# Performance work log

Measured on AMD Instinct MI355X. Metric: run time of the kernel, lower is better.

Reference implementation:

```python
import jax, jax.numpy as jnp
import numpy as np

DIM, M_DIM, FOURIER, KNN = 128, 16, 4, 32
EDGE_IN = 2 * FOURIER + 2 * DIM + 1  # 265


def silu(x):
    return x * jax.nn.sigmoid(x)


def setup_inputs() -> dict:
    key = jax.random.key(0)
    ks = jax.random.split(key, 12)
    b, n = 2, 4096

    def w(k, shape):
        return jax.random.normal(k, shape, dtype=jnp.float32) * 0.02

    return {
        "feats": jax.random.normal(ks[0], (b, n, DIM), dtype=jnp.float32),
        "coors": jax.random.normal(ks[1], (b, n, 3), dtype=jnp.float32) * 3.0,
        # edge_mlp: Linear(265, 530) -> SiLU -> Linear(530, 16) -> SiLU
        "We1": w(ks[2], (EDGE_IN, 2 * EDGE_IN)), "be1": jnp.zeros((2 * EDGE_IN,), jnp.float32),
        "We2": w(ks[3], (2 * EDGE_IN, M_DIM)), "be2": jnp.zeros((M_DIM,), jnp.float32),
        # coors_mlp: Linear(16, 64) -> SiLU -> Linear(64, 1)
        "Wc1": w(ks[4], (M_DIM, 4 * M_DIM)), "bc1": jnp.zeros((4 * M_DIM,), jnp.float32),
        "Wc2": w(ks[5], (4 * M_DIM, 1)), "bc2": jnp.zeros((1,), jnp.float32),
        # node_mlp: Linear(dim+16, 2*dim) -> SiLU -> Linear(2*dim, dim)
        "Wn1": w(ks[6], (DIM + M_DIM, 2 * DIM)), "bn1": jnp.zeros((2 * DIM,), jnp.float32),
        "Wn2": w(ks[7], (2 * DIM, DIM)), "bn2": jnp.zeros((DIM,), jnp.float32),
    }


def reference(feats, coors, We1, be1, We2, be2, Wc1, bc1, Wc2, bc2, Wn1, bn1, Wn2, bn2):
    b, n, d = feats.shape
    # pairwise relative coords and squared distance: (b, n, n, 3), (b, n, n)
    rel_coors = coors[:, :, None, :] - coors[:, None, :, :]
    rel_dist = jnp.sum(rel_coors ** 2, axis=-1)

    # k nearest neighbors (smallest distance)
    _, idx = jax.lax.top_k(-rel_dist, KNN)  # (b, n, K)
    rel_coors = jnp.take_along_axis(rel_coors, idx[..., None], axis=2)  # (b, n, K, 3)
    rel_dist = jnp.take_along_axis(rel_dist, idx, axis=2)[..., None]    # (b, n, K, 1)

    # fourier encode distance -> (b, n, K, 2*F + 1)
    scales = 2.0 ** jnp.arange(FOURIER, dtype=rel_dist.dtype)
    xs = rel_dist[..., None] / scales  # (b, n, K, 1, F)
    fe = jnp.concatenate([jnp.sin(xs), jnp.cos(xs), rel_dist[..., None]], axis=-1)
    rel_dist = fe.reshape(b, n, KNN, 2 * FOURIER + 1)

    bidx = jnp.arange(b)[:, None, None]
    feats_j = feats[bidx, idx]                                   # (b, n, K, d)
    feats_i = jnp.broadcast_to(feats[:, :, None, :], (b, n, KNN, d))

    edge_in = jnp.concatenate([feats_i, feats_j, rel_dist], axis=-1)  # (b, n, K, 265)
    m_ij = silu(silu(edge_in @ We1 + be1) @ We2 + be2)                # (b, n, K, m)

    coor_w = (silu(m_ij @ Wc1 + bc1) @ Wc2 + bc2)[..., 0]             # (b, n, K)
    coors_out = jnp.einsum('bij,bijc->bic', coor_w, rel_coors) + coors

    m_i = m_ij.sum(axis=2)                                            # (b, n, m)
    node_h = silu(jnp.concatenate([feats, m_i], axis=-1) @ Wn1 + bn1)
    node_out = node_h @ Wn2 + bn2 + feats
    return node_out, coors_out
```

## Files before the change

kernel.cpp:

```cpp
#include <hip/hip_runtime.h>
#include <hip/hip_bf16.h>
#include <stdint.h>

typedef __hip_bfloat16 bf16;

using sh8    = __attribute__((ext_vector_type(8)))  short;
using sh4    = __attribute__((ext_vector_type(4)))  short;
using us4    = __attribute__((ext_vector_type(4)))  unsigned short;
using f32x16 = __attribute__((ext_vector_type(16))) float;
using fx4    = __attribute__((ext_vector_type(4)))  float;

#define NN    4096
#define NODES 8192
#define DIM   128
#define MD    16
#define KNNK  32
#define H1N   530
#define CPAD  544
#define PROW  1088

#define OFF_W1AB 0
#define OFF_WE2A 8704
#define OFF_WC1A 17536
#define OFF_BE2  19584
#define OFF_BC1  19616
#define OFF_WC2  19744
#define OFF_BC2  19872
#define WIMG_SH  19880

__device__ __forceinline__ float b2f(bf16 x){ return __bfloat162float(x); }
__device__ __forceinline__ bf16  f2b(float x){ return __float2bfloat16(x); }
__device__ __forceinline__ float silu_f(float x){
    return x * __builtin_amdgcn_rcpf(1.f + __expf(-x));
}

__device__ __forceinline__ unsigned short f2us(float f){
    unsigned x = __float_as_uint(f);
    unsigned r = x + 0x7FFFu + ((x >> 16) & 1u);
    return (unsigned short)(r >> 16);
}
__device__ __forceinline__ float us2f(unsigned short u){
    return __uint_as_float(((unsigned)u) << 16);
}
__device__ __forceinline__ unsigned pkbf(float a, float b){
    __hip_bfloat162 v = __float22bfloat162_rn(make_float2(a, b));
    return *(unsigned*)&v;
}

struct Ptrs { const void* p[14]; int n[14]; };

__global__ __launch_bounds__(256) void detect_kernel(Ptrs ps, int* flags){
    int tn = blockIdx.x;
    const bf16* s = (const bf16*)ps.p[tn];
    int n = ps.n[tn]; if (n > 8192) n = 8192;
    int bad = 0;
    for (int i = threadIdx.x; i < n; i += 256){
        float v = b2f(s[i]);
        if (!(fabsf(v) <= 64.f)) bad = 1;
    }
    __shared__ int sbad;
    if (threadIdx.x == 0) sbad = 0;
    __syncthreads();
    if (bad) atomicOr(&sbad, 1);
    __syncthreads();
    if (threadIdx.x == 0) flags[tn] = sbad;
}

struct ConvTab {
    const void* src[14];
    int dstoff[14];
    int prefix[15];
};

__global__ __launch_bounds__(256) void convert_all(ConvTab tab,
                                                   const int* __restrict__ flags,
                                                   float* __restrict__ base){
    int gid = blockIdx.x * 256 + threadIdx.x;
    if (gid >= tab.prefix[14]) return;
    int tn = 0;
    #pragma unroll
    for (int k = 1; k < 14; ++k)
        if (gid >= tab.prefix[k]) tn = k;
    int local = gid - tab.prefix[tn];
    int f = flags[tn];
    float v = f ? ((const float*)tab.src[tn])[local]
                : b2f(((const bf16*)tab.src[tn])[local]);
    base[tab.dstoff[tn] + local] = v;
}

__global__ __launch_bounds__(256) void prep_kernel(
        const float* __restrict__ We1, const float* __restrict__ We2,
        const float* __restrict__ Wc1, const float* __restrict__ be2,
        const float* __restrict__ bc1, const float* __restrict__ Wc2,
        const float* __restrict__ bc2, const float* __restrict__ feats,
        unsigned short* __restrict__ gwimg,
        unsigned short* __restrict__ We1T,
        unsigned short* __restrict__ fBF){
    int gid = blockIdx.x * 256 + threadIdx.x;
    if (gid < 4352){
        int c = gid >> 3, f = gid & 7;
        gwimg[OFF_W1AB + gid] = (c < H1N) ? f2us(We1[(size_t)(256 + f) * H1N + c]) : 0;
    } else if (gid < 8704){
        int e = gid - 4352; int c = e >> 3, jj = e & 7;
        gwimg[OFF_W1AB + 4352 + e] =
            (jj == 0 && c < H1N) ? f2us(We1[(size_t)264 * H1N + c]) : 0;
    } else if (gid < 17536){
        int e = gid - 8704; int o = e / 552, c = e - o * 552;
        gwimg[OFF_WE2A + e] = (c < H1N) ? f2us(We2[(size_t)c * 16 + o]) : 0;
    } else if (gid < 19584){
        int e = gid - 17536; int u = e >> 5, k = e & 31;
        gwimg[OFF_WC1A + e] = (k < 16) ? f2us(Wc1[(size_t)k * 64 + u]) : 0;
    } else if (gid < 19600){
        ((float*)(gwimg + OFF_BE2))[gid - 19584] = be2[gid - 19584];
    } else if (gid < 19664){
        ((float*)(gwimg + OFF_BC1))[gid - 19600] = bc1[gid - 19600];
    } else if (gid < 19728){
        ((float*)(gwimg + OFF_WC2))[gid - 19664] = Wc2[gid - 19664];
    } else if (gid < 19732){
        int z = gid - 19728;
        ((float*)(gwimg + OFF_BC2))[z] = (z == 0) ? bc2[0] : 0.f;
    } else if (gid >= 32768 && gid < 32768 + 1088 * 128){
        int e = gid - 32768; int n = e >> 7, k = e & 127;
        float v;
        if (n < CPAD) v = (n < H1N) ? We1[(size_t)k * H1N + n] : 0.f;
        else { int n2 = n - CPAD; v = (n2 < H1N) ? We1[(size_t)(128 + k) * H1N + n2] : 0.f; }
        We1T[e] = f2us(v);
    } else if (gid >= 172032 && gid < 172032 + NODES * DIM){
        int e = gid - 172032;
        fBF[e] = f2us(feats[e]);
    }
}

__global__ __launch_bounds__(256) void knn_kernel(const float* __restrict__ coors,
                                                  int* __restrict__ idx_out){
    __shared__ unsigned hist[4][1024];
    __shared__ unsigned sBin, sBelow;
    __shared__ unsigned wpart[4];
    __shared__ int  sOcnt;
    __shared__ unsigned long long wred64[4];
    __shared__ unsigned long long sWin64;

    int node = blockIdx.x;
    int b = node >> 12, i = node & (NN - 1);
    const float* cb = coors + (size_t)b * NN * 3;
    int t = threadIdx.x, lane = t & 63, wid = t >> 6;

    float qx = cb[i*3+0], qy = cb[i*3+1], qz = cb[i*3+2];

    unsigned db[16];
    unsigned bk[16];
    #pragma unroll
    for (int s = 0; s < 16; ++s){
        int j = (s << 8) + t;
        float dx = qx - cb[j*3+0];
        float dy = qy - cb[j*3+1];
        float dz = qz - cb[j*3+2];
        float d  = dx*dx + dy*dy + dz*dz;
        float d2 = d * d;
        db[s] = __float_as_uint(d);
        bk[s] = __float_as_uint(d2 * d2) >> 22;
    }

    {
        uint4* hz = (uint4*)hist;
        uint4 z = make_uint4(0,0,0,0);
        #pragma unroll
        for (int e = 0; e < 4; ++e) hz[e * 256 + t] = z;
    }
    __syncthreads();
    #pragma unroll
    for (int s = 0; s < 16; ++s)
        atomicAdd(&hist[wid][bk[s]], 1u);
    if (t == 0) sOcnt = 0;
    __syncthreads();

    unsigned cnt[4]; unsigned S = 0;
    #pragma unroll
    for (int r = 0; r < 4; ++r){
        unsigned c = hist[0][4*t+r] + hist[1][4*t+r] + hist[2][4*t+r] + hist[3][4*t+r];
        cnt[r] = c; S += c;
    }
    unsigned scan = S;
    #pragma unroll
    for (int off = 1; off < 64; off <<= 1){
        unsigned nv = __shfl_up(scan, off);
        if (lane >= off) scan += nv;
    }
    if (lane == 63) wpart[wid] = scan;
    __syncthreads();
    unsigned wbase = 0;
    #pragma unroll
    for (int w = 0; w < 4; ++w)
        if (w < wid) wbase += wpart[w];
    unsigned run = wbase + scan - S;
    #pragma unroll
    for (int r = 0; r < 4; ++r){
        if (run < KNNK && run + cnt[r] >= KNNK){ sBin = 4*t + r; sBelow = run; }
        run += cnt[r];
    }
    __syncthreads();
    unsigned B = sBin, need = KNNK - sBelow;

    #pragma unroll
    for (int s = 0; s < 16; ++s){
        if (bk[s] < B){
            int pos = atomicAdd(&sOcnt, 1);
            idx_out[(size_t)node * KNNK + pos] = (s << 8) + t;
        }
    }
    __syncthreads();
    int C = sOcnt;
    unsigned long long lastk = 0;
    for (unsigned r = 0; r < need; ++r){
        unsigned long long lmin = ~0ull;
        #pragma unroll
        for (int s = 0; s < 16; ++s){
            if (bk[s] == B){
                unsigned long long mk =
                    (((unsigned long long)db[s] << 32) | (unsigned)((s << 8) + t)) + 1ull;
                if (mk > lastk && mk < lmin) lmin = mk;
            }
        }
        #pragma unroll
        for (int off = 32; off > 0; off >>= 1){
            unsigned long long o = __shfl_xor(lmin, off);
            if (o < lmin) lmin = o;
        }
        if (lane == 0) wred64[wid] = lmin;
        __syncthreads();
        if (t == 0){
            unsigned long long m = wred64[0];
            if (wred64[1] < m) m = wred64[1];
            if (wred64[2] < m) m = wred64[2];
            if (wred64[3] < m) m = wred64[3];
            sWin64 = m;
            idx_out[(size_t)node * KNNK + C + r] = (int)(unsigned)((m - 1ull) & 0xffffffffull);
        }
        __syncthreads();
        lastk = sWin64;
    }
}

__global__ __launch_bounds__(256) void p_gemm(const unsigned short* __restrict__ fBF,
                                              const unsigned short* __restrict__ We1T,
                                              const float* __restrict__ be1,
                                              unsigned short* __restrict__ P){
    int t = threadIdx.x, lane = t & 63, wid = t >> 6;
    int e31 = lane & 31, hi = lane >> 5;
    int mW = (blockIdx.x << 7) + (wid << 5);
    int n0 = blockIdx.y << 5;

    const unsigned short* Arow = fBF  + (size_t)(mW + e31) * DIM + hi * 8;
    const unsigned short* Brow = We1T + (size_t)(n0 + e31) * DIM + hi * 8;

    f32x16 acc = {0.f,0.f,0.f,0.f,0.f,0.f,0.f,0.f,0.f,0.f,0.f,0.f,0.f,0.f,0.f,0.f};
    #pragma unroll
    for (int kc = 0; kc < 8; ++kc){
        sh8 a  = *(const sh8*)(Arow + kc * 16);
        sh8 bv = *(const sh8*)(Brow + kc * 16);
        acc = __builtin_amdgcn_mfma_f32_32x32x16_bf16(a, bv, acc, 0, 0, 0);
    }
    int n = n0 + e31;
    float beadd = 0.f;
    if (n < CPAD) beadd = (n < H1N) ? be1[n] : 0.f;
    #pragma unroll
    for (int g = 0; g < 4; ++g)
        #pragma unroll
        for (int r = 0; r < 4; ++r){
            int m = mW + 8*g + 4*hi + r;
            P[(size_t)m * PROW + n] = f2us(acc[4*g + r] + beadd);
        }
}

__global__ __launch_bounds__(512, 6) void edge_kernel(
        const float* __restrict__ coors, const int* __restrict__ idx,
        const unsigned short* __restrict__ gw,
        const unsigned short* __restrict__ P,
        float* __restrict__ mi_out, void* __restrict__ dout,
        const int* __restrict__ flagp){
    __shared__ __align__(16) unsigned short sWe2[16 * 552];
    __shared__ __align__(16) unsigned short trans[8][1280];

    int t = threadIdx.x, lane = t & 63, wid = t >> 6;
    int gnode = (blockIdx.x << 3) + wid;
    int b = gnode >> 12;

    {
        const float4* s1 = (const float4*)(gw + OFF_WE2A);
        float4* d1 = (float4*)sWe2;
        for (int e = t; e < 1104; e += 512) d1[e] = s1[e];
    }

    const float* cb = coors + (size_t)b * NN * 3;
    int i = gnode & (NN - 1);
    float qx = cb[i*3+0], qy = cb[i*3+1], qz = cb[i*3+2];

    int e31 = lane & 31, hi = lane >> 5;
    int e15 = lane & 15, q  = lane >> 4;

    int jme = idx[(size_t)gnode * KNNK + e31];
    float rx = qx - cb[jme*3+0];
    float ry = qy - cb[jme*3+1];
    float rz = qz - cb[jme*3+2];
    float d = rx*rx + ry*ry + rz*rz;

    unsigned frb[9];
    frb[0] = f2us(sinf(d));         frb[1] = f2us(sinf(d * 0.5f));
    frb[2] = f2us(sinf(d * 0.25f)); frb[3] = f2us(sinf(d * 0.125f));
    frb[4] = f2us(cosf(d));         frb[5] = f2us(cosf(d * 0.5f));
    frb[6] = f2us(cosf(d * 0.25f)); frb[7] = f2us(cosf(d * 0.125f));
    frb[8] = f2us(d);

    sh8 bfragC;
    #pragma unroll
    for (int j = 0; j < 8; ++j)
        bfragC[j] = (hi == 0) ? (short)frb[j]
                  : (short)((j == 0) ? frb[8] : (j == 1) ? 0x3F80u : 0u);

    int nbase = gnode & ~(NN - 1);
    int j0 = __shfl(jme, lane >> 2);
    int j1 = __shfl(jme, 16 + (lane >> 2));
    const unsigned short* Pst0 = P + (size_t)(nbase + j0) * PROW + CPAD + (lane & 3) * 8;
    const unsigned short* Pst1 = P + (size_t)(nbase + j1) * PROW + CPAD + (lane & 3) * 8;
    const unsigned short* Pirow = P + (size_t)gnode * PROW;

    unsigned short* stg = &trans[wid][0];
    unsigned short* sw0 = stg + (lane >> 2) * 40 + (lane & 3) * 8;
    unsigned short* sw1 = stg + (16 + (lane >> 2)) * 40 + (lane & 3) * 8;

    const float* g_be2 = (const float*)(gw + OFF_BE2);
    const float* g_bc1 = (const float*)(gw + OFF_BC1);
    const float* g_wc2 = (const float*)(gw + OFF_WC2);
    const float* g_bc2 = (const float*)(gw + OFF_BC2);

    fx4 accD0 = {0.f,0.f,0.f,0.f};
    fx4 accD1 = {0.f,0.f,0.f,0.f};

    __syncthreads();

    for (int ch = 0; ch < 17; ++ch){
        int c0 = ch * 32;
        sh8 g0v = *(const sh8*)(Pst0 + c0);
        sh8 g1v = *(const sh8*)(Pst1 + c0);
        unsigned short piS = Pirow[c0 + e31];
        sh8 afrag = *(const sh8*)(gw + OFF_W1AB + (size_t)(hi * 544 + c0 + e31) * 8);
        afrag[1] = hi ? (short)piS : afrag[1];

        *(sh8*)sw0 = g0v;
        *(sh8*)sw1 = g1v;
        asm volatile("s_waitcnt lgkmcnt(0)" ::: "memory");

        f32x16 cc;
        #pragma unroll
        for (int g = 0; g < 4; ++g){
            us4 pj = *(const us4*)(stg + e31 * 40 + 8*g + 4*hi);
            cc[4*g+0] = us2f(pj.x);
            cc[4*g+1] = us2f(pj.y);
            cc[4*g+2] = us2f(pj.z);
            cc[4*g+3] = us2f(pj.w);
        }
        f32x16 h = __builtin_amdgcn_mfma_f32_32x32x16_bf16(afrag, bfragC, cc, 0, 0, 0);

        #pragma unroll
        for (int g = 0; g < 4; ++g){
            unsigned lo = pkbf(silu_f(h[4*g+0]), silu_f(h[4*g+1]));
            unsigned hi2 = pkbf(silu_f(h[4*g+2]), silu_f(h[4*g+3]));
            *(uint2*)&stg[e31 * 40 + 8*g + 4*hi] = make_uint2(lo, hi2);
        }
        asm volatile("s_waitcnt lgkmcnt(0)" ::: "memory");

        sh8 wa  = *(const sh8*)&sWe2[e15 * 552 + c0 + q * 8];
        sh8 bt0 = *(const sh8*)&stg[e15 * 40 + q * 8];
        sh8 bt1 = *(const sh8*)&stg[(16 + e15) * 40 + q * 8];
        accD0 = __builtin_amdgcn_mfma_f32_16x16x32_bf16(wa, bt0, accD0, 0, 0, 0);
        accD1 = __builtin_amdgcn_mfma_f32_16x16x32_bf16(wa, bt1, accD1, 0, 0, 0);
    }

    fx4 be2q = *(const fx4*)&g_be2[q * 4];
    float msum[4];
    float mv0[4], mv1[4];
    #pragma unroll
    for (int r = 0; r < 4; ++r){
        mv0[r] = silu_f(accD0[r] + be2q[r]);
        mv1[r] = silu_f(accD1[r] + be2q[r]);
        msum[r] = mv0[r] + mv1[r];
    }
    *(uint2*)&stg[e15 * 16 + q * 4] =
        make_uint2(pkbf(mv0[0], mv0[1]), pkbf(mv0[2], mv0[3]));
    *(uint2*)&stg[(16 + e15) * 16 + q * 4] =
        make_uint2(pkbf(mv1[0], mv1[1]), pkbf(mv1[2], mv1[3]));
    #pragma unroll
    for (int r = 0; r < 4; ++r){
        msum[r] += __shfl_xor(msum[r], 1);
        msum[r] += __shfl_xor(msum[r], 2);
        msum[r] += __shfl_xor(msum[r], 4);
        msum[r] += __shfl_xor(msum[r], 8);
    }
    if (e15 == 0){
        fx4 mv = { msum[0], msum[1], msum[2], msum[3] };
        *(fx4*)(mi_out + (size_t)gnode * MD + q * 4) = mv;
    }
    asm volatile("s_waitcnt lgkmcnt(0)" ::: "memory");

    float tsum0 = 0.f, tsum1 = 0.f;
    #pragma unroll
    for (int ut = 0; ut < 4; ++ut){
        sh8 wa3 = *(const sh8*)(gw + OFF_WC1A + (size_t)(ut * 16 + e15) * 32 + q * 8);
        sh8 b0  = (q < 2) ? *(const sh8*)&stg[e15 * 16 + q * 8]        : (sh8)0;
        sh8 b1  = (q < 2) ? *(const sh8*)&stg[(16 + e15) * 16 + q * 8] : (sh8)0;
        fx4 a0 = {0.f,0.f,0.f,0.f};
        fx4 a1 = {0.f,0.f,0.f,0.f};
        a0 = __builtin_amdgcn_mfma_f32_16x16x32_bf16(wa3, b0, a0, 0, 0, 0);
        a1 = __builtin_amdgcn_mfma_f32_16x16x32_bf16(wa3, b1, a1, 0, 0, 0);
        fx4 bc1q = *(const fx4*)&g_bc1[ut * 16 + q * 4];
        fx4 wcq  = *(const fx4*)&g_wc2[ut * 16 + q * 4];
        #pragma unroll
        for (int r = 0; r < 4; ++r){
            tsum0 += silu_f(a0[r] + bc1q[r]) * wcq[r];
            tsum1 += silu_f(a1[r] + bc1q[r]) * wcq[r];
        }
    }
    tsum0 += __shfl_xor(tsum0, 16); tsum0 += __shfl_xor(tsum0, 32);
    tsum1 += __shfl_xor(tsum1, 16); tsum1 += __shfl_xor(tsum1, 32);
    float cw = ((lane < 16) ? tsum0 : tsum1) + g_bc2[0];

    float en = (lane < 32) ? 1.f : 0.f;
    float cx = en * cw * rx, cy = en * cw * ry, cz = en * cw * rz;
    #pragma unroll
    for (int off = 1; off <= 32; off <<= 1){
        cx += __shfl_xor(cx, off);
        cy += __shfl_xor(cy, off);
        cz += __shfl_xor(cz, off);
    }
    if (lane == 0){
        size_t base = (size_t)NODES * DIM + (size_t)gnode * 3;
        if (*flagp){
            float* o = (float*)dout;
            o[base+0] = cx + qx; o[base+1] = cy + qy; o[base+2] = cz + qz;
        } else {
            bf16* o = (bf16*)dout;
            o[base+0] = f2b(cx + qx); o[base+1] = f2b(cy + qy); o[base+2] = f2b(cz + qz);
        }
    }
}

__global__ __launch_bounds__(256) void node_kernel(
        const float* __restrict__ feats, const float* __restrict__ m_i,
        const float* __restrict__ Wn1,   const float* __restrict__ bn1,
        const float* __restrict__ Wn2,   const float* __restrict__ bn2,
        void* __restrict__ dout,         const int* __restrict__ flagp){
    __shared__ float X[8][144];
    __shared__ float Hs[8][256];
    int t = threadIdx.x;
    int g0 = blockIdx.x << 3;

    for (int e = t; e < 8 * DIM; e += 256){
        int nd = e >> 7, c = e & 127;
        X[nd][c] = feats[(size_t)(g0 + nd) * DIM + c];
    }
    if (t < 128){
        int nd = t >> 4, c = t & 15;
        X[nd][DIM + c] = m_i[(size_t)(g0 + nd) * MD + c];
    }
    __syncthreads();

    float acc[8] = {};
    for (int r = 0; r < 144; ++r){
        float w = Wn1[(size_t)r * 256 + t];
        #pragma unroll
        for (int nd = 0; nd < 8; ++nd) acc[nd] += X[nd][r] * w;
    }
    float bb = bn1[t];
    #pragma unroll
    for (int nd = 0; nd < 8; ++nd) Hs[nd][t] = silu_f(acc[nd] + bb);
    __syncthreads();

    int c = t & 127, g = t >> 7;
    float a2[4] = {};
    for (int r = 0; r < 256; ++r){
        float w = Wn2[(size_t)r * DIM + c];
        #pragma unroll
        for (int u = 0; u < 4; ++u) a2[u] += Hs[g*4 + u][r] * w;
    }
    float b2v = bn2[c];
    int fl = *flagp;
    #pragma unroll
    for (int u = 0; u < 4; ++u){
        int nd = g*4 + u;
        float v = a2[u] + b2v + X[nd][c];
        size_t off2 = (size_t)(g0 + nd) * DIM + c;
        if (fl) ((float*)dout)[off2] = v;
        else    ((bf16*)dout)[off2]  = f2b(v);
    }
}

extern "C" void kernel_launch(void* const* d_in, const int* in_sizes, int n_in,
                              void* d_out, int out_size, void* d_ws, size_t ws_size,
                              hipStream_t stream){
    char* ws = (char*)d_ws;
    size_t off = 0;
    auto alloc = [&](size_t bytes) -> char* {
        off = (off + 511) & ~(size_t)511;
        char* p = ws + off;
        off += bytes;
        return p;
    };

    int* flags = (int*)alloc(14 * 4);

    ConvTab tab;
    int total = 0;
    for (int i = 0; i < 14; ++i){ tab.prefix[i] = total; total += in_sizes[i]; }
    tab.prefix[14] = total;
    float* convBase = (float*)alloc((size_t)total * 4);
    int doff = 0;
    for (int i = 0; i < 14; ++i){
        tab.src[i] = d_in[i];
        tab.dstoff[i] = doff;
        doff += in_sizes[i];
    }

    unsigned short* gwimg = (unsigned short*)alloc((size_t)WIMG_SH * 2);
    unsigned short* We1T  = (unsigned short*)alloc((size_t)1088 * 128 * 2);
    unsigned short* fBF   = (unsigned short*)alloc((size_t)NODES * DIM * 2);
    int*   idx    = (int*)  alloc((size_t)NODES * KNNK * 4);
    unsigned short* P = (unsigned short*) alloc((size_t)NODES * PROW * 2);
    float* mi     = (float*)alloc((size_t)NODES * MD * 4);

    Ptrs ps;
    for (int i = 0; i < 14; ++i){ ps.p[i] = d_in[i]; ps.n[i] = in_sizes[i]; }
    detect_kernel<<<14, 256, 0, stream>>>(ps, flags);
    convert_all<<<(total + 255) / 256, 256, 0, stream>>>(tab, flags, convBase);

    const float* feats = convBase + tab.dstoff[0];
    const float* coors = convBase + tab.dstoff[1];
    const float* We1 = convBase + tab.dstoff[2],  * be1 = convBase + tab.dstoff[3];
    const float* We2 = convBase + tab.dstoff[4],  * be2 = convBase + tab.dstoff[5];
    const float* Wc1 = convBase + tab.dstoff[6],  * bc1 = convBase + tab.dstoff[7];
    const float* Wc2 = convBase + tab.dstoff[8],  * bc2 = convBase + tab.dstoff[9];
    const float* Wn1 = convBase + tab.dstoff[10], * bn1 = convBase + tab.dstoff[11];
    const float* Wn2 = convBase + tab.dstoff[12], * bn2 = convBase + tab.dstoff[13];

    prep_kernel<<<(172032 + NODES * DIM) / 256, 256, 0, stream>>>(
        We1, We2, Wc1, be2, bc1, Wc2, bc2, feats, gwimg, We1T, fBF);
    knn_kernel<<<NODES, 256, 0, stream>>>(coors, idx);
    p_gemm<<<dim3(64, 34), 256, 0, stream>>>(fBF, We1T, be1, P);
    edge_kernel<<<NODES/8, 512, 0, stream>>>(coors, idx, gwimg, P, mi,
                                             d_out, flags + 0);
    node_kernel<<<1024, 256, 0, stream>>>(feats, mi, Wn1, bn1, Wn2, bn2,
                                          d_out, flags + 0);
}
```

Before: 263.0 us.

## Restructure KNN to one wavefront per query node with per-wave histogram selection

```diff
diff --git a/kernel.cpp b/kernel.cpp
--- a/kernel.cpp
+++ b/kernel.cpp
@@ -131,113 +131,145 @@
     }
 }
 
-__global__ __launch_bounds__(256) void knn_kernel(const float* __restrict__ coors,
-                                                  int* __restrict__ idx_out){
-    __shared__ unsigned hist[4][1024];
-    __shared__ unsigned sBin, sBelow;
-    __shared__ unsigned wpart[4];
-    __shared__ int  sOcnt;
-    __shared__ unsigned long long wred64[4];
-    __shared__ unsigned long long sWin64;
-
-    int node = blockIdx.x;
+__global__ __launch_bounds__(512, 6) void knn_kernel(const float* __restrict__ coors,
+                                                     int* __restrict__ idx_out){
+    __shared__ unsigned hist[8][1024];
+    __shared__ unsigned long long blist[8][64];
+    __shared__ int cntO[8], cntB[8];
+
+    int t = threadIdx.x, lane = t & 63, wid = t >> 6;
+    int node = (blockIdx.x << 3) + wid;
     int b = node >> 12, i = node & (NN - 1);
     const float* cb = coors + (size_t)b * NN * 3;
-    int t = threadIdx.x, lane = t & 63, wid = t >> 6;
 
     float qx = cb[i*3+0], qy = cb[i*3+1], qz = cb[i*3+2];
 
-    unsigned db[16];
-    unsigned bk[16];
-    #pragma unroll
-    for (int s = 0; s < 16; ++s){
-        int j = (s << 8) + t;
-        float dx = qx - cb[j*3+0];
-        float dy = qy - cb[j*3+1];
-        float dz = qz - cb[j*3+2];
-        float d  = dx*dx + dy*dy + dz*dz;
-        float d2 = d * d;
-        db[s] = __float_as_uint(d);
-        bk[s] = __float_as_uint(d2 * d2) >> 22;
-    }
-
+    unsigned* h = &hist[wid][0];
     {
-        uint4* hz = (uint4*)hist;
+        uint4* hz = (uint4*)h;
         uint4 z = make_uint4(0,0,0,0);
         #pragma unroll
-        for (int e = 0; e < 4; ++e) hz[e * 256 + t] = z;
-    }
-    __syncthreads();
-    #pragma unroll
-    for (int s = 0; s < 16; ++s)
-        atomicAdd(&hist[wid][bk[s]], 1u);
-    if (t == 0) sOcnt = 0;
-    __syncthreads();
-
-    unsigned cnt[4]; unsigned S = 0;
-    #pragma unroll
-    for (int r = 0; r < 4; ++r){
-        unsigned c = hist[0][4*t+r] + hist[1][4*t+r] + hist[2][4*t+r] + hist[3][4*t+r];
-        cnt[r] = c; S += c;
-    }
+        for (int zl = 0; zl < 4; ++zl) hz[zl * 64 + lane] = z;
+    }
+    if (lane == 0){ cntO[wid] = 0; cntB[wid] = 0; }
+    asm volatile("" ::: "memory");
+
+    unsigned bkp[32];
+    #pragma unroll
+    for (int so = 0; so < 8; ++so){
+        #pragma unroll
+        for (int si = 0; si < 8; ++si){
+            int s = so * 8 + si;
+            int j = (s << 6) + lane;
+            float dx = qx - cb[j*3+0];
+            float dy = qy - cb[j*3+1];
+            float dz = qz - cb[j*3+2];
+            float d  = dx*dx + dy*dy + dz*dz;
+            float d2 = d * d;
+            unsigned bk = __float_as_uint(d2 * d2) >> 22;
+            if ((s & 1) == 0) bkp[s >> 1] = bk;
+            else              bkp[s >> 1] |= bk << 16;
+            atomicAdd(&h[bk], 1u);
+        }
+        asm volatile("" ::: "memory");
+    }
+    asm volatile("s_waitcnt lgkmcnt(0)" ::: "memory");
+
+    unsigned c16[16];
+    {
+        uint4* hz = (uint4*)h;
+        #pragma unroll
+        for (int g = 0; g < 4; ++g){
+            uint4 v = hz[lane * 4 + g];
+            c16[g*4+0] = v.x; c16[g*4+1] = v.y; c16[g*4+2] = v.z; c16[g*4+3] = v.w;
+        }
+    }
+    unsigned S = 0;
+    #pragma unroll
+    for (int r = 0; r < 16; ++r) S += c16[r];
     unsigned scan = S;
     #pragma unroll
     for (int off = 1; off < 64; off <<= 1){
         unsigned nv = __shfl_up(scan, off);
         if (lane >= off) scan += nv;
     }
-    if (lane == 63) wpart[wid] = scan;
-    __syncthreads();
-    unsigned wbase = 0;
-    #pragma unroll
-    for (int w = 0; w < 4; ++w)
-        if (w < wid) wbase += wpart[w];
-    unsigned run = wbase + scan - S;
-    #pragma unroll
-    for (int r = 0; r < 4; ++r){
-        if (run < KNNK && run + cnt[r] >= KNNK){ sBin = 4*t + r; sBelow = run; }
-        run += cnt[r];
-    }
-    __syncthreads();
-    unsigned B = sBin, need = KNNK - sBelow;
-
-    #pragma unroll
-    for (int s = 0; s < 16; ++s){
-        if (bk[s] < B){
-            int pos = atomicAdd(&sOcnt, 1);
-            idx_out[(size_t)node * KNNK + pos] = (s << 8) + t;
-        }
-    }
-    __syncthreads();
-    int C = sOcnt;
-    unsigned long long lastk = 0;
-    for (unsigned r = 0; r < need; ++r){
-        unsigned long long lmin = ~0ull;
-        #pragma unroll
-        for (int s = 0; s < 16; ++s){
-            if (bk[s] == B){
-                unsigned long long mk =
-                    (((unsigned long long)db[s] << 32) | (unsigned)((s << 8) + t)) + 1ull;
-                if (mk > lastk && mk < lmin) lmin = mk;
+    unsigned excl = scan - S;
+    unsigned long long own = __ballot(excl < KNNK && excl + S >= KNNK);
+    int src = __ffsll((unsigned long long)own) - 1;
+    unsigned run = excl, Bloc = 0, below_l = 0;
+    #pragma unroll
+    for (int r = 0; r < 16; ++r){
+        if (run < KNNK && run + c16[r] >= KNNK){ Bloc = lane * 16 + r; below_l = run; }
+        run += c16[r];
+    }
+    unsigned B    = __shfl(Bloc, src);
+    unsigned below= __shfl(below_l, src);
+    unsigned need = KNNK - below;
+
+    int* co = &cntO[wid];
+    int* cbn = &cntB[wid];
+    unsigned long long* bl = &blist[wid][0];
+    #pragma unroll
+    for (int s = 0; s < 64; ++s){
+        unsigned bk = (bkp[s >> 1] >> ((s & 1) * 16)) & 0xffffu;
+        int j = (s << 6) + lane;
+        if (bk < B){
+            int pos = atomicAdd(co, 1);
+            idx_out[(size_t)node * KNNK + pos] = j;
+        } else if (bk == B){
+            float dx = qx - cb[j*3+0];
+            float dy = qy - cb[j*3+1];
+            float dz = qz - cb[j*3+2];
+            float d  = dx*dx + dy*dy + dz*dz;
+            unsigned long long mk = ((unsigned long long)__float_as_uint(d) << 32)
+                                    | (unsigned)j;
+            int p = atomicAdd(cbn, 1);
+            if (p < 64) bl[p] = mk;
+        }
+    }
+    asm volatile("s_waitcnt lgkmcnt(0) vmcnt(0)" ::: "memory");
+    int nb = *cbn;
+
+    if (nb <= 64){
+        unsigned long long e = (lane < nb) ? bl[lane] : ~0ull;
+        for (unsigned r = 0; r < need; ++r){
+            unsigned long long m = e;
+            #pragma unroll
+            for (int off = 32; off > 0; off >>= 1){
+                unsigned long long o = __shfl_xor(m, off);
+                if (o < m) m = o;
             }
-        }
-        #pragma unroll
-        for (int off = 32; off > 0; off >>= 1){
-            unsigned long long o = __shfl_xor(lmin, off);
-            if (o < lmin) lmin = o;
-        }
-        if (lane == 0) wred64[wid] = lmin;
-        __syncthreads();
-        if (t == 0){
-            unsigned long long m = wred64[0];
-            if (wred64[1] < m) m = wred64[1];
-            if (wred64[2] < m) m = wred64[2];
-            if (wred64[3] < m) m = wred64[3];
-            sWin64 = m;
-            idx_out[(size_t)node * KNNK + C + r] = (int)(unsigned)((m - 1ull) & 0xffffffffull);
-        }
-        __syncthreads();
-        lastk = sWin64;
+            if (lane == 0)
+                idx_out[(size_t)node * KNNK + below + r] = (int)(unsigned)(m & 0xffffffffull);
+            if (e == m) e = ~0ull;
+        }
+    } else {
+        unsigned long long lastk = 0;
+        for (unsigned r = 0; r < need; ++r){
+            unsigned long long lmin = ~0ull;
+            for (int s = 0; s < 64; ++s){
+                int j = (s << 6) + lane;
+                float dx = qx - cb[j*3+0];
+                float dy = qy - cb[j*3+1];
+                float dz = qz - cb[j*3+2];
+                float d  = dx*dx + dy*dy + dz*dz;
+                float d2 = d * d;
+                if ((__float_as_uint(d2 * d2) >> 22) == B){
+                    unsigned long long mk = (((unsigned long long)__float_as_uint(d) << 32)
+                                             | (unsigned)j) + 1ull;
+                    if (mk > lastk && mk < lmin) lmin = mk;
+                }
+            }
+            #pragma unroll
+            for (int off = 32; off > 0; off >>= 1){
+                unsigned long long o = __shfl_xor(lmin, off);
+                if (o < lmin) lmin = o;
+            }
+            if (lane == 0)
+                idx_out[(size_t)node * KNNK + below + r] =
+                    (int)(unsigned)((lmin - 1ull) & 0xffffffffull);
+            lastk = lmin;
+        }
     }
 }
 
@@ -543,7 +575,7 @@
 
     prep_kernel<<<(172032 + NODES * DIM) / 256, 256, 0, stream>>>(
         We1, We2, Wc1, be2, bc1, Wc2, bc2, feats, gwimg, We1T, fBF);
-    knn_kernel<<<NODES, 256, 0, stream>>>(coors, idx);
+    knn_kernel<<<NODES/8, 512, 0, stream>>>(coors, idx);
     p_gemm<<<dim3(64, 34), 256, 0, stream>>>(fBF, We1T, be1, P);
     edge_kernel<<<NODES/8, 512, 0, stream>>>(coors, idx, gwimg, P, mi,
                                              d_out, flags + 0);
```

Result: slower. 425.3 us (+61.7%).
